# Performance work log

Measured on AMD Instinct MI355X. Metric: run time of the kernel, lower is better.

The kernel has to match this reference:

```python
import jax, jax.numpy as jnp
import numpy as np

H = 8          # num_heads
EPS = 1e-6     # layernorm epsilon
NEG_INF = -1e9


def _ln(x, g, b):
    m = jnp.mean(x, axis=-1, keepdims=True)
    v = jnp.mean(jnp.square(x - m), axis=-1, keepdims=True)
    return g * (x - m) * jax.lax.rsqrt(v + EPS) + b


def _mha(xq, kv, wq, wk, wv, wo, bias):
    # xq: [B,Tq,D], kv: [B,Tk,D]; weights [D,D]. Returns (out [B,Tq,D], weights [B,H,Tq,Tk]).
    B, Tq, D = xq.shape
    dh = D // H
    q = (xq @ wq) * (dh ** -0.5)
    k = kv @ wk
    v = kv @ wv
    q = q.reshape(B, Tq, H, dh).transpose(0, 2, 1, 3)
    k = k.reshape(B, -1, H, dh).transpose(0, 2, 1, 3)
    v = v.reshape(B, -1, H, dh).transpose(0, 2, 1, 3)
    logits = jnp.einsum('bhqd,bhkd->bhqk', q, k)
    if bias is not None:
        logits = logits + bias
    w = jax.nn.softmax(logits, axis=-1)
    out = jnp.einsum('bhqk,bhkd->bhqd', w, v).transpose(0, 2, 1, 3).reshape(B, Tq, D)
    return out @ wo, w


def setup_inputs() -> dict:
    key = jax.random.key(0)
    ks = jax.random.split(key, 16)
    B, Td, Te, D, F, L = 2, 2048, 2048, 512, 2048, 2
    s = 0.02
    inp = {
        'x': jax.random.normal(ks[0], (B, Td, D), jnp.float32),
        'enc_a': jax.random.normal(ks[1], (B, Te, D), jnp.float32),
        'enc_c': jax.random.normal(ks[2], (B, Te, D), jnp.float32),
        'sa_wq': jax.random.normal(ks[3], (L, D, D), jnp.float32) * s,
        'sa_wk': jax.random.normal(ks[4], (L, D, D), jnp.float32) * s,
        'sa_wv': jax.random.normal(ks[5], (L, D, D), jnp.float32) * s,
        'sa_wo': jax.random.normal(ks[6], (L, D, D), jnp.float32) * s,
        'ed_wq': jax.random.normal(ks[7], (L, D, D), jnp.float32) * s,
        'ed_wk': jax.random.normal(ks[8], (L, D, D), jnp.float32) * s,
        'ed_wv': jax.random.normal(ks[9], (L, D, D), jnp.float32) * s,
        'ed_wo': jax.random.normal(ks[10], (L, D, D), jnp.float32) * s,
        'ffn_w1': jax.random.normal(ks[11], (L, D, F), jnp.float32) * s,
        'ffn_w2': jax.random.normal(ks[12], (L, F, D), jnp.float32) * s,
        'ln1_g': jnp.ones((L, D), jnp.float32), 'ln1_b': jnp.zeros((L, D), jnp.float32),
        'ln2_g': jnp.ones((L, D), jnp.float32), 'ln2_b': jnp.zeros((L, D), jnp.float32),
        'ln3_g': jnp.ones((L, D), jnp.float32), 'ln3_b': jnp.zeros((L, D), jnp.float32),
        'out_g': jnp.ones((D,), jnp.float32), 'out_b': jnp.zeros((D,), jnp.float32),
    }
    return inp


def reference(x, enc_a, enc_c, sa_wq, sa_wk, sa_wv, sa_wo, ed_wq, ed_wk, ed_wv, ed_wo,
              ffn_w1, ffn_w2, ln1_g, ln1_b, ln2_g, ln2_b, ln3_g, ln3_b, out_g, out_b):
    B, T, D = x.shape
    L = sa_wq.shape[0]
    # decoder self-attention causal bias, broadcast over [B,H]
    causal = jnp.where(jnp.tril(jnp.ones((T, T), bool)), 0.0, NEG_INF)[None, None]
    avg = None
    for i in range(L):
        h = _ln(x, ln1_g[i], ln1_b[i])
        y, _ = _mha(h, h, sa_wq[i], sa_wk[i], sa_wv[i], sa_wo[i], causal)
        x = x + y  # residual (dropout inactive at eval)
        h = _ln(x, ln2_g[i], ln2_b[i])
        y0, _ = _mha(h, enc_a, ed_wq[i], ed_wk[i], ed_wv[i], ed_wo[i], None)
        y1, w = _mha(h, enc_c, ed_wq[i], ed_wk[i], ed_wv[i], ed_wo[i], None)
        # original overwrites attn_scores with second call's head-averaged weights
        scores = jnp.mean(w, axis=1) / L
        avg = scores if avg is None else avg + scores
        x = x + y0 + y1
        h = _ln(x, ln3_g[i], ln3_b[i])
        x = x + jax.nn.relu(h @ ffn_w1[i]) @ ffn_w2[i]
    x = _ln(x, out_g, out_b)
    return x, avg
```

## Files before the change

kernel.cpp:

```cpp
#include <hip/hip_runtime.h>
#include <hip/hip_bf16.h>

#define BB 2
#define TT 2048
#define DD 512
#define FF 2048
#define HH 8
#define DH 64
#define LL 2
#define MM (BB*TT)

typedef __attribute__((ext_vector_type(8))) short bf16x8;
typedef __attribute__((ext_vector_type(4))) float f32x4;

__device__ __forceinline__ float bf2f(unsigned short u) {
    return __uint_as_float(((unsigned int)u) << 16);
}
__device__ __forceinline__ unsigned short f2bf(float f) {
    unsigned int u = __float_as_uint(f);
    u += 0x7fffu + ((u >> 16) & 1u);
    return (unsigned short)(u >> 16);
}
__device__ __forceinline__ unsigned int cvtpk(float a, float b) {
    unsigned int r;
    asm("v_cvt_pk_bf16_f32 %0, %1, %2" : "=v"(r) : "v"(a), "v"(b));
    return r;
}
__device__ __forceinline__ void gload16(const void* g, void* l) {
    __builtin_amdgcn_global_load_lds((__attribute__((address_space(1))) void*)g,
                                     (__attribute__((address_space(3))) void*)l, 16, 0, 0);
}

template<bool BF16OUT>
__global__ __launch_bounds__(256) void ln_kernel(const float* __restrict__ x,
                                                 const float* __restrict__ g,
                                                 const float* __restrict__ b,
                                                 void* __restrict__ out)
{
    const int row = blockIdx.x;
    const int tid = threadIdx.x;
    const float2 v = ((const float2*)(x + (size_t)row * DD))[tid];
    float s = v.x + v.y;
    float q = v.x * v.x + v.y * v.y;
    #pragma unroll
    for (int off = 32; off; off >>= 1) {
        s += __shfl_down(s, off);
        q += __shfl_down(q, off);
    }
    __shared__ float ss[4], qq[4];
    const int wid = tid >> 6;
    if ((tid & 63) == 0) { ss[wid] = s; qq[wid] = q; }
    __syncthreads();
    s = ss[0] + ss[1] + ss[2] + ss[3];
    q = qq[0] + qq[1] + qq[2] + qq[3];
    const float mean = s * (1.0f / DD);
    const float var = q * (1.0f / DD) - mean * mean;
    const float inv = rsqrtf(var + 1e-6f);
    const float2 gg = ((const float2*)g)[tid];
    const float2 bb = ((const float2*)b)[tid];
    const float ox = gg.x * (v.x - mean) * inv + bb.x;
    const float oy = gg.y * (v.y - mean) * inv + bb.y;
    if (BF16OUT) {
        const unsigned int pk = cvtpk(ox, oy);
        ((unsigned int*)((unsigned short*)out + (size_t)row * DD))[tid] = pk;
    } else {
        float2 o; o.x = ox; o.y = oy;
        ((float2*)((float*)out + (size_t)row * DD))[tid] = o;
    }
}

struct CvtEJob { const float* s; unsigned short* d; };
struct CvtEJobs2 { CvtEJob j[2]; };

__global__ __launch_bounds__(256) void cvt_kernel(CvtEJobs2 P, int n)
{
    const CvtEJob jb = P.j[blockIdx.z];
    const int i = (blockIdx.x * 256 + threadIdx.x) * 8;
    if (i >= n) return;
    const float4 a = *(const float4*)(jb.s + i);
    const float4 b = *(const float4*)(jb.s + i + 4);
    unsigned int o[4];
    o[0] = cvtpk(a.x, a.y); o[1] = cvtpk(a.z, a.w);
    o[2] = cvtpk(b.x, b.y); o[3] = cvtpk(b.z, b.w);
    *(bf16x8*)(jb.d + i) = *(bf16x8*)o;
}

struct CvtTJob { const float* s; unsigned short* d; int K; int N; };
struct CvtTJobs20 { CvtTJob j[20]; };

__global__ __launch_bounds__(256) void cvtT_kernel(CvtTJobs20 P)
{
    __shared__ float t[32][33];
    const CvtTJob jb = P.j[blockIdx.z];
    const int gk = blockIdx.y << 5, gn = blockIdx.x << 5;
    if (gk >= jb.K || gn >= jb.N) return;
    const int tx = threadIdx.x & 31, ty = threadIdx.x >> 5;
    #pragma unroll
    for (int i = 0; i < 4; ++i)
        t[ty + i * 8][tx] = jb.s[(size_t)(gk + ty + i * 8) * jb.N + gn + tx];
    __syncthreads();
    #pragma unroll
    for (int i = 0; i < 4; ++i)
        jb.d[(size_t)(gn + ty + i * 8) * jb.K + gk + tx] = f2bf(t[tx][ty + i * 8]);
}

struct GemmJob {
    const unsigned short* A;
    const unsigned short* Wt;
    const float* res;
    float* Cf;
    unsigned short* Cb;
    unsigned short* Ct;
    float scale;
    int relu;
};
struct GemmJobs8 { GemmJob j[8]; };

__global__ __launch_bounds__(256, 2) void gemm_mfma(GemmJobs8 P, int M, int N, int K)
{
    __shared__ __align__(16) unsigned char lds[32768];
    const GemmJob jb = P.j[blockIdx.z];
    const int tid = threadIdx.x, lane = tid & 63, w = tid >> 6;
    const int bn = blockIdx.x << 7, bm = blockIdx.y << 7;
    const int wr = (w >> 1) << 6, wc = (w & 1) << 6;
    const size_t strA = (size_t)K * 2;

    f32x4 acc[4][4] = {};
    const int akey = (lane & 7) << 4;
    const int frow = lane & 15;
    const int kq = (lane >> 4) << 4;

    for (int kt = 0; kt < K; kt += 64) {
        __syncthreads();
        #pragma unroll
        for (int c = 0; c < 4; ++c) {
            const int q = c * 4 + w;
            const int o = (q << 10) + (lane << 4);
            const int row = o >> 7;
            const int colb = (o & 127) ^ ((row & 7) << 4);
            gload16((const char*)jb.A + (size_t)(bm + row) * strA + kt * 2 + colb,
                    lds + (q << 10));
            gload16((const char*)jb.Wt + (size_t)(bn + row) * strA + kt * 2 + colb,
                    lds + 16384 + (q << 10));
        }
        asm volatile("s_waitcnt vmcnt(0)" ::: "memory");
        __syncthreads();
        #pragma unroll
        for (int kk = 0; kk < 2; ++kk) {
            bf16x8 av[4], bv[4];
            #pragma unroll
            for (int i = 0; i < 4; ++i) {
                const int rA = wr + (i << 4) + frow;
                av[i] = *(const bf16x8*)(lds + (rA << 7) + ((((kk << 6) + kq)) ^ akey));
                const int rB = wc + (i << 4) + frow;
                bv[i] = *(const bf16x8*)(lds + 16384 + (rB << 7) + ((((kk << 6) + kq)) ^ akey));
            }
            #pragma unroll
            for (int i = 0; i < 4; ++i)
                #pragma unroll
                for (int j = 0; j < 4; ++j)
                    acc[i][j] = __builtin_amdgcn_mfma_f32_16x16x32_bf16(av[i], bv[j], acc[i][j], 0, 0, 0);
        }
    }

    const int crow0 = (lane >> 4) << 2;
    const int ccol = lane & 15;
    if (jb.Ct) {
        #pragma unroll
        for (int i = 0; i < 4; ++i)
            #pragma unroll
            for (int j = 0; j < 4; ++j) {
                const int gm = bm + wr + (i << 4) + crow0;
                const int gn = bn + wc + (j << 4) + ccol;
                const int bI = gm >> 11, t = gm & 2047;
                const int hI = gn >> 6, d = gn & 63;
                uint2 pk;
                pk.x = cvtpk(acc[i][j][0], acc[i][j][1]);
                pk.y = cvtpk(acc[i][j][2], acc[i][j][3]);
                *(uint2*)(jb.Ct + ((size_t)((bI * HH + hI) * DH + d)) * TT + t) = pk;
            }
        return;
    }
    #pragma unroll
    for (int i = 0; i < 4; ++i) {
        #pragma unroll
        for (int j = 0; j < 4; ++j) {
            #pragma unroll
            for (int r = 0; r < 4; ++r) {
                const int gm = bm + wr + (i << 4) + crow0 + r;
                const int gn = bn + wc + (j << 4) + ccol;
                float v = acc[i][j][r] * jb.scale;
                if (jb.relu) v = fmaxf(v, 0.f);
                const size_t idx = (size_t)gm * N + gn;
                if (jb.res) v += jb.res[idx];
                if (jb.Cf) jb.Cf[idx] = v;
                if (jb.Cb) jb.Cb[idx] = f2bf(v);
            }
        }
    }
}

template<bool CAUSAL, bool DUAL, int NQ>
__global__ __launch_bounds__(256, (NQ == 1) ? 4 : 3) void flash_mfma(
    const unsigned short* __restrict__ q,
    const unsigned short* __restrict__ ka, const unsigned short* __restrict__ vta,
    const unsigned short* __restrict__ kc, const unsigned short* __restrict__ vtc,
    unsigned short* __restrict__ Opart,
    float* __restrict__ mlpart)
{
    __shared__ __align__(16) char lds[(NQ == 1) ? 40960 : 49152];
    const int tid = threadIdx.x;
    const int lane = tid & 63, w = tid >> 6;
    const int g4 = lane >> 4, c = lane & 15;

    constexpr int GX = (32 / NQ) * 2;
    const int f = blockIdx.x + GX * (blockIdx.y + 8 * blockIdx.z);
    const int xcd = f & 7;
    const int tt = f >> 3;
    const int u = tt % GX;
    const int half = u & 1, jq = u >> 1;
    const int grp = (tt / GX) * 8 + xcd;
    int b, h, which;
    if (DUAL) { which = grp & 1; b = (grp >> 1) & 1; h = grp >> 2; }
    else      { which = 0;       b = grp & 1;        h = grp >> 1; }
    const int q0 = jq * (64 * NQ);
    const int q0w = q0 + w * (16 * NQ);
    const int kendw = q0w + 16 * NQ;

    const unsigned short* k  = (DUAL && which) ? kc : ka;
    const unsigned short* vt = (DUAL && which) ? vtc : vta;
    const int slot = (DUAL ? (which << 1) : 0) + half;
    unsigned short* Od = Opart + (size_t)slot * MM * DD;
    float* mld = mlpart + (size_t)slot * (BB * HH * TT * 2);

    bf16x8 Qf[NQ][2];
    #pragma unroll
    for (int jb = 0; jb < NQ; ++jb) {
        const unsigned short* qp = q + (size_t)(b * TT + q0w + (jb << 4) + c) * DD + h * DH + (g4 << 3);
        Qf[jb][0] = *(const bf16x8*)qp;
        Qf[jb][1] = *(const bf16x8*)(qp + 32);
    }
    const char* kbase = (const char*)(k + (size_t)b * TT * DD + h * DH);
    const char* vtb   = (const char*)(vt + (size_t)(b * HH + h) * DH * TT);
    char* Pw = lds + 32768 + w * (NQ * 2048);
    const int pkey = (c & 7) << 4;

    f32x4 O[NQ][4] = {};
    float lpart[NQ];
    #pragma unroll
    for (int jb = 0; jb < NQ; ++jb) lpart[jb] = 0.f;

    const int ntt = CAUSAL ? ((q0 + 64 * NQ) >> 6) : (TT >> 6);
    const int tBeg = half ? ((ntt + 1) >> 1) : 0;
    const int tEnd = half ? ntt : ((ntt + 1) >> 1);

    auto STAGE = [&](int t, int sel) {
        const int kt = t << 6;
        char* Kb = lds + sel * 8192;
        char* Vb = lds + 16384 + sel * 8192;
        #pragma unroll
        for (int c8 = 0; c8 < 2; ++c8) {
            const int qc = (c8 << 2) + w;
            const int o = (qc << 10) + (lane << 4);
            const int row = o >> 7;
            const int colb = (o & 127) ^ ((row & 7) << 4);
            gload16(kbase + (size_t)(kt + row) * (DD * 2) + colb, Kb + (qc << 10));
            gload16(vtb + (size_t)row * (TT * 2) + kt * 2 + colb, Vb + (qc << 10));
        }
    };

    if (tBeg < tEnd) {
        STAGE(tBeg, 0);
        asm volatile("s_waitcnt vmcnt(0)" ::: "memory");
        __syncthreads();

        for (int t = tBeg; t < tEnd; ++t) {
            const int cur = (t - tBeg) & 1;
            if (t + 1 < tEnd) STAGE(t + 1, cur ^ 1);
            const int kt = t << 6;

            if (!CAUSAL || kt < kendw) {
                const char* Kb = lds + cur * 8192;
                const char* Vb = lds + 16384 + cur * 8192;

                f32x4 s[NQ][4] = {};
                #pragma unroll
                for (int kk = 0; kk < 2; ++kk) {
                    bf16x8 av[4];
                    #pragma unroll
                    for (int i = 0; i < 4; ++i) {
                        const int r = (i << 4) + c;
                        av[i] = *(const bf16x8*)(Kb + (r << 7) + (((kk << 6) + (g4 << 4)) ^ ((r & 7) << 4)));
                    }
                    #pragma unroll
                    for (int i = 0; i < 4; ++i)
                        #pragma unroll
                        for (int jb = 0; jb < NQ; ++jb)
                            s[jb][i] = __builtin_amdgcn_mfma_f32_16x16x32_bf16(av[i], Qf[jb][kk], s[jb][i], 0, 0, 0);
                }

                #pragma unroll
                for (int jb = 0; jb < NQ; ++jb) {
                    const int qbase = q0w + (jb << 4);
                    if (CAUSAL && kt + 63 > qbase) {
                        #pragma unroll
                        for (int i = 0; i < 4; ++i)
                            #pragma unroll
                            for (int r = 0; r < 4; ++r)
                                if (kt + (i << 4) + (g4 << 2) + r > qbase + c) s[jb][i][r] = -1e30f;
                    }
                    float ps = 0.f;
                    #pragma unroll
                    for (int i = 0; i < 4; ++i)
                        #pragma unroll
                        for (int r = 0; r < 4; ++r) {
                            const float p = exp2f(s[jb][i][r]);
                            s[jb][i][r] = p;
                            ps += p;
                        }
                    lpart[jb] += ps;
                    #pragma unroll
                    for (int i = 0; i < 4; ++i) {
                        uint2 pk;
                        pk.x = cvtpk(s[jb][i][0], s[jb][i][1]);
                        pk.y = cvtpk(s[jb][i][2], s[jb][i][3]);
                        const int baddr = (((jb << 4) + c) << 7) + (((i << 4) + (g4 << 2)) << 1);
                        *(uint2*)(Pw + (baddr ^ pkey)) = pk;
                    }
                }
                asm volatile("s_waitcnt lgkmcnt(0)" ::: "memory");
                __builtin_amdgcn_sched_barrier(0);

                #pragma unroll
                for (int kk = 0; kk < 2; ++kk) {
                    bf16x8 pa[NQ];
                    #pragma unroll
                    for (int jb = 0; jb < NQ; ++jb)
                        pa[jb] = *(const bf16x8*)(Pw + (((((jb << 4) + c) << 7) + (kk << 6) + (g4 << 4)) ^ pkey));
                    #pragma unroll
                    for (int jj = 0; jj < 4; ++jj) {
                        const int d = (jj << 4) + c;
                        const bf16x8 vb = *(const bf16x8*)(Vb + (d << 7) + (((kk << 6) + (g4 << 4)) ^ ((d & 7) << 4)));
                        #pragma unroll
                        for (int jb = 0; jb < NQ; ++jb)
                            O[jb][jj] = __builtin_amdgcn_mfma_f32_16x16x32_bf16(pa[jb], vb, O[jb][jj], 0, 0, 0);
                    }
                }
            }

            asm volatile("s_waitcnt vmcnt(0)" ::: "memory");
            __syncthreads();
        }
    }

    #pragma unroll
    for (int jb = 0; jb < NQ; ++jb) {
        float l2 = lpart[jb] + __shfl_xor(lpart[jb], 16);
        const float ltot = l2 + __shfl_xor(l2, 32);
        #pragma unroll
        for (int jj = 0; jj < 4; ++jj)
            #pragma unroll
            for (int r = 0; r < 4; ++r) {
                const int qr = q0w + (jb << 4) + (g4 << 2) + r;
                Od[(size_t)(b * TT + qr) * DD + h * DH + (jj << 4) + c] = f2bf(O[jb][jj][r]);
            }
        if (lane < 16) {
            const size_t mi = (((size_t)b * HH + h) * TT + q0w + (jb << 4) + lane) * 2;
            mld[mi] = 0.f;
            mld[mi + 1] = ltot;
        }
    }
}

template<int NS>
__global__ __launch_bounds__(256) void merge_kernel(
    const unsigned short* __restrict__ Opart, const float* __restrict__ mlpart,
    unsigned short* __restrict__ out)
{
    const int row = blockIdx.x;
    const int b = row >> 11, rt = row & 2047;
    const int t = threadIdx.x;
    const int d0 = t << 1, h = d0 >> 6;
    float acc0 = 0.f, acc1 = 0.f;
    #pragma unroll
    for (int s = 0; s < NS; ++s) {
        const size_t mb = ((size_t)(b * HH + h) * TT + rt) * 2;
        const float* mp0 = mlpart + (size_t)(s * 2 + 0) * (BB * HH * TT * 2) + mb;
        const float* mp1 = mlpart + (size_t)(s * 2 + 1) * (BB * HH * TT * 2) + mb;
        const float m0 = mp0[0], l0 = mp0[1], m1 = mp1[0], l1 = mp1[1];
        const float M = fmaxf(m0, m1);
        const float a0 = exp2f(m0 - M), a1 = exp2f(m1 - M);
        const float inv = 1.f / (a0 * l0 + a1 * l1);
        const unsigned short* p0 = Opart + (size_t)(s * 2 + 0) * MM * DD + (size_t)row * DD + d0;
        const unsigned short* p1 = Opart + (size_t)(s * 2 + 1) * MM * DD + (size_t)row * DD + d0;
        acc0 += (a0 * bf2f(p0[0]) + a1 * bf2f(p1[0])) * inv;
        acc1 += (a0 * bf2f(p0[1]) + a1 * bf2f(p1[1])) * inv;
    }
    ((unsigned int*)(out + (size_t)row * DD))[t] = cvtpk(acc0, acc1);
}

__global__ __launch_bounds__(256) void avg_mfma_kernel(const unsigned short* __restrict__ qm,
                                                       const unsigned short* __restrict__ kcm,
                                                       const float* __restrict__ mlpart,
                                                       float* __restrict__ avg, int first)
{
    __shared__ __align__(16) unsigned char ldsQ[8192];
    __shared__ __align__(16) unsigned char ldsK[4][8192];
    __shared__ float sM[8][64];
    __shared__ float sIL[8][64];
    const int tid = threadIdx.x;
    const int lane = tid & 63, w = tid >> 6;

    const int f = blockIdx.x;
    const int xcd = f & 7, t = f >> 3;
    const int b = xcd >> 2;
    const int q0 = ((((xcd & 3) << 3) + (t >> 3))) << 6;
    const int kt0 = (((t & 7) << 2) + w) << 6;

    #pragma unroll
    for (int u = 0; u < 2; ++u) {
        const int e = (u << 8) + tid;
        const int h = e >> 6, r = e & 63;
        const size_t mb = ((size_t)(b * HH + h) * TT + q0 + r) * 2;
        const float* mp2 = mlpart + (size_t)2 * (BB * HH * TT * 2) + mb;
        const float* mp3 = mlpart + (size_t)3 * (BB * HH * TT * 2) + mb;
        const float m2 = mp2[0], l2v = mp2[1], m3 = mp3[0], l3v = mp3[1];
        const float M = fmaxf(m2, m3);
        const float L = exp2f(m2 - M) * l2v + exp2f(m3 - M) * l3v;
        sM[h][r] = M;
        sIL[h][r] = 1.f / L;
    }

    float avac[4][4][4] = {};
    const int akey = (lane & 7) << 4;
    const int frow = lane & 15;
    const int kq = (lane >> 4) << 4;
    const int crow0 = (lane >> 4) << 2;

    for (int h = 0; h < 8; ++h) {
        __syncthreads();
        #pragma unroll
        for (int u = 0; u < 2; ++u) {
            const int ch = (u << 2) + w;
            const int o = (ch << 10) + (lane << 4);
            const int row = o >> 7;
            const int colb = (o & 127) ^ ((row & 7) << 4);
            gload16((const char*)qm + ((size_t)(b * TT + q0 + row) * DD + h * DH) * 2 + colb,
                    ldsQ + (ch << 10));
        }
        #pragma unroll
        for (int c8 = 0; c8 < 8; ++c8) {
            const int o = (c8 << 10) + (lane << 4);
            const int row = o >> 7;
            const int colb = (o & 127) ^ ((row & 7) << 4);
            gload16((const char*)kcm + ((size_t)(b * TT + kt0 + row) * DD + h * DH) * 2 + colb,
                    &ldsK[w][c8 << 10]);
        }
        asm volatile("s_waitcnt vmcnt(0)" ::: "memory");
        __syncthreads();

        f32x4 s[4][4] = {};
        #pragma unroll
        for (int kk = 0; kk < 2; ++kk) {
            bf16x8 qv[4], kv[4];
            #pragma unroll
            for (int i = 0; i < 4; ++i) {
                qv[i] = *(const bf16x8*)(ldsQ + (((i << 4) + frow) << 7) + (((kk << 6) + kq) ^ akey));
                kv[i] = *(const bf16x8*)(&ldsK[w][(((i << 4) + frow) << 7) + (((kk << 6) + kq) ^ akey)]);
            }
            #pragma unroll
            for (int i = 0; i < 4; ++i)
                #pragma unroll
                for (int j = 0; j < 4; ++j)
                    s[i][j] = __builtin_amdgcn_mfma_f32_16x16x32_bf16(qv[i], kv[j], s[i][j], 0, 0, 0);
        }
        #pragma unroll
        for (int i = 0; i < 4; ++i)
            #pragma unroll
            for (int j = 0; j < 4; ++j)
                #pragma unroll
                for (int r = 0; r < 4; ++r) {
                    const int qr = (i << 4) + crow0 + r;
                    avac[i][j][r] += exp2f(s[i][j][r] - sM[h][qr]) * sIL[h][qr];
                }
    }

    float* dst = avg + ((size_t)b * TT + q0) * TT + kt0;
    #pragma unroll
    for (int i = 0; i < 4; ++i)
        #pragma unroll
        for (int j = 0; j < 4; ++j)
            #pragma unroll
            for (int r = 0; r < 4; ++r) {
                const int qr = (i << 4) + crow0 + r;
                const int kc = (j << 4) + (lane & 15);
                const float v = avac[i][j][r] * (1.f / (HH * LL));
                float* p = dst + (size_t)qr * TT + kc;
                *p = first ? v : (*p + v);
            }
}

extern "C" void kernel_launch(void* const* d_in, const int* in_sizes, int n_in,
                              void* d_out, int out_size, void* d_ws, size_t ws_size,
                              hipStream_t stream)
{
    const float* x_in   = (const float*)d_in[0];
    const float* enc_a  = (const float*)d_in[1];
    const float* enc_c  = (const float*)d_in[2];
    const float* sa_wq0 = (const float*)d_in[3];
    const float* sa_wk0 = (const float*)d_in[4];
    const float* sa_wv0 = (const float*)d_in[5];
    const float* sa_wo0 = (const float*)d_in[6];
    const float* ed_wq0 = (const float*)d_in[7];
    const float* ed_wk0 = (const float*)d_in[8];
    const float* ed_wv0 = (const float*)d_in[9];
    const float* ed_wo0 = (const float*)d_in[10];
    const float* ffn_w10 = (const float*)d_in[11];
    const float* ffn_w20 = (const float*)d_in[12];
    const float* ln1_g0 = (const float*)d_in[13];
    const float* ln1_b0 = (const float*)d_in[14];
    const float* ln2_g0 = (const float*)d_in[15];
    const float* ln2_b0 = (const float*)d_in[16];
    const float* ln3_g0 = (const float*)d_in[17];
    const float* ln3_b0 = (const float*)d_in[18];
    const float* out_g  = (const float*)d_in[19];
    const float* out_b  = (const float*)d_in[20];

    const size_t NTD = (size_t)MM * DD;
    const size_t MB = 1u << 20;
    char* W = (char*)d_ws;
    float*          x_buf   = (float*)(W);
    unsigned short* h_bf    = (unsigned short*)(W + 8 * MB);
    unsigned short* q_bf    = (unsigned short*)(W + 12 * MB);
    unsigned short* k1_bf   = (unsigned short*)(W + 16 * MB);
    unsigned short* vt1     = (unsigned short*)(W + 20 * MB);
    unsigned short* k2_bf   = (unsigned short*)(W + 24 * MB);
    unsigned short* vt2     = (unsigned short*)(W + 28 * MB);
    unsigned short* attnA   = (unsigned short*)(W + 32 * MB);
    unsigned short* attnS   = (unsigned short*)(W + 36 * MB);
    unsigned short* encA_bf = (unsigned short*)(W + 41 * MB);
    unsigned short* encC_bf = (unsigned short*)(W + 45 * MB);
    unsigned short* wbf     = (unsigned short*)(W + 49 * MB);
    unsigned short* Opart   = (unsigned short*)(W + 68 * MB);
    float*          mlpart  = (float*)(W + 84 * MB);
    unsigned short* ffn_bf  = q_bf;

    unsigned short* w1t = wbf + (size_t)16 * DD * DD;
    unsigned short* w2t = w1t + (size_t)2 * DD * FF;
    auto wd = [&](int l, int which) { return wbf + ((size_t)(l * 8 + which)) * DD * DD; };

    float* x_out   = (float*)d_out;
    float* avg_out = (float*)d_out + NTD;

    hipMemcpyAsync(x_buf, x_in, NTD * sizeof(float), hipMemcpyDeviceToDevice, stream);

    {
        CvtTJobs20 J{};
        const float* srcs[8] = {sa_wq0, sa_wk0, sa_wv0, sa_wo0, ed_wq0, ed_wk0, ed_wv0, ed_wo0};
        for (int l = 0; l < LL; ++l)
            for (int t = 0; t < 8; ++t)
                J.j[l * 8 + t] = {srcs[t] + (size_t)l * DD * DD, wd(l, t), DD, DD};
        for (int l = 0; l < LL; ++l) {
            J.j[16 + l] = {ffn_w10 + (size_t)l * DD * FF, w1t + (size_t)l * FF * DD, DD, FF};
            J.j[18 + l] = {ffn_w20 + (size_t)l * FF * DD, w2t + (size_t)l * DD * FF, FF, DD};
        }
        cvtT_kernel<<<dim3(FF / 32, FF / 32, 20), 256, 0, stream>>>(J);
    }
    {
        CvtEJobs2 J{};
        J.j[0] = {enc_a, encA_bf};
        J.j[1] = {enc_c, encC_bf};
        cvt_kernel<<<dim3(NTD / 8 / 256, 1, 2), 256, 0, stream>>>(J, (int)NTD);
    }

    const dim3 flashSelfG(64, HH, BB);
    const dim3 flashCrossG(32, HH, BB * 2);
    const float qscale = 0.125f * 1.4426950408889634f;

    for (int i = 0; i < LL; ++i) {
        const size_t fOff = (size_t)i * DD * FF;
        const size_t lOff = (size_t)i * DD;

        ln_kernel<true><<<MM, 256, 0, stream>>>(x_buf, ln1_g0 + lOff, ln1_b0 + lOff, h_bf);
        {
            GemmJobs8 J{};
            J.j[0] = {h_bf, wd(i, 0), nullptr, nullptr, q_bf, nullptr, qscale, 0};
            J.j[1] = {h_bf, wd(i, 1), nullptr, nullptr, k1_bf, nullptr, 1.f, 0};
            J.j[2] = {h_bf, wd(i, 2), nullptr, nullptr, nullptr, vt1, 1.f, 0};
            gemm_mfma<<<dim3(DD / 128, MM / 128, 3), 256, 0, stream>>>(J, MM, DD, DD);
        }
        flash_mfma<true, false, 1><<<flashSelfG, 256, 0, stream>>>(
            q_bf, k1_bf, vt1, nullptr, nullptr, Opart, mlpart);
        merge_kernel<1><<<MM, 256, 0, stream>>>(Opart, mlpart, attnA);
        {
            GemmJobs8 J{};
            J.j[0] = {attnA, wd(i, 3), x_buf, x_buf, nullptr, nullptr, 1.f, 0};
            gemm_mfma<<<dim3(DD / 128, MM / 128, 1), 256, 0, stream>>>(J, MM, DD, DD);
        }

        ln_kernel<true><<<MM, 256, 0, stream>>>(x_buf, ln2_g0 + lOff, ln2_b0 + lOff, h_bf);
        {
            GemmJobs8 J{};
            J.j[0] = {h_bf,    wd(i, 4), nullptr, nullptr, q_bf, nullptr, qscale, 0};
            J.j[1] = {encA_bf, wd(i, 5), nullptr, nullptr, k1_bf, nullptr, 1.f, 0};
            J.j[2] = {encA_bf, wd(i, 6), nullptr, nullptr, nullptr, vt1, 1.f, 0};
            J.j[3] = {encC_bf, wd(i, 5), nullptr, nullptr, k2_bf, nullptr, 1.f, 0};
            J.j[4] = {encC_bf, wd(i, 6), nullptr, nullptr, nullptr, vt2, 1.f, 0};
            gemm_mfma<<<dim3(DD / 128, MM / 128, 5), 256, 0, stream>>>(J, MM, DD, DD);
        }
        flash_mfma<false, true, 2><<<flashCrossG, 256, 0, stream>>>(
            q_bf, k1_bf, vt1, k2_bf, vt2, Opart, mlpart);
        merge_kernel<2><<<MM, 256, 0, stream>>>(Opart, mlpart, attnS);
        avg_mfma_kernel<<<512, 256, 0, stream>>>(q_bf, k2_bf, mlpart, avg_out, (i == 0) ? 1 : 0);
        {
            GemmJobs8 J{};
            J.j[0] = {attnS, wd(i, 7), x_buf, x_buf, nullptr, nullptr, 1.f, 0};
            gemm_mfma<<<dim3(DD / 128, MM / 128, 1), 256, 0, stream>>>(J, MM, DD, DD);
        }

        ln_kernel<true><<<MM, 256, 0, stream>>>(x_buf, ln3_g0 + lOff, ln3_b0 + lOff, h_bf);
        {
            GemmJobs8 J{};
            J.j[0] = {h_bf, w1t + fOff, nullptr, nullptr, ffn_bf, nullptr, 1.f, 1};
            gemm_mfma<<<dim3(FF / 128, MM / 128, 1), 256, 0, stream>>>(J, MM, FF, DD);
        }
        {
            GemmJobs8 J{};
            J.j[0] = {ffn_bf, w2t + fOff, x_buf, x_buf, nullptr, nullptr, 1.f, 0};
            gemm_mfma<<<dim3(DD / 128, MM / 128, 1), 256, 0, stream>>>(J, MM, DD, FF);
        }
    }

    ln_kernel<false><<<MM, 256, 0, stream>>>(x_buf, out_g, out_b, x_out);
}
```

Measured before the change: 663.7 us.

## Split head-averaged attention kernel across head groups with atomic accumulation

Restructures the attention-weight averaging kernel from 512 blocks of four waves into 4096 single-wave blocks. Each block now handles one 64x64 query/key tile for a group of four heads, so the block-wide barriers and shared Q staging across waves go away. Partial results from the two head groups and the two layers are combined with float atomic adds into an output that is zeroed once up front with a memset. This raises parallelism and removes the first-layer branch, at the cost of a 32MB memset, doubled atomic traffic to the output, and reloading Q separately per wave.

```diff
diff --git a/kernel.cpp b/kernel.cpp
--- a/kernel.cpp
+++ b/kernel.cpp
@@ -399,36 +399,38 @@
     ((unsigned int*)(out + (size_t)row * DD))[t] = cvtpk(acc0, acc1);
 }
 
-__global__ __launch_bounds__(256) void avg_mfma_kernel(const unsigned short* __restrict__ qm,
-                                                       const unsigned short* __restrict__ kcm,
-                                                       const float* __restrict__ mlpart,
-                                                       float* __restrict__ avg, int first)
+__global__ __launch_bounds__(64) void avg_mfma_kernel(const unsigned short* __restrict__ qm,
+                                                      const unsigned short* __restrict__ kcm,
+                                                      const float* __restrict__ mlpart,
+                                                      float* __restrict__ avg)
 {
     __shared__ __align__(16) unsigned char ldsQ[8192];
-    __shared__ __align__(16) unsigned char ldsK[4][8192];
-    __shared__ float sM[8][64];
-    __shared__ float sIL[8][64];
-    const int tid = threadIdx.x;
-    const int lane = tid & 63, w = tid >> 6;
+    __shared__ __align__(16) unsigned char ldsK[8192];
+    __shared__ float sM[4][64];
+    __shared__ float sIL[4][64];
+    const int lane = threadIdx.x;
 
     const int f = blockIdx.x;
-    const int xcd = f & 7, t = f >> 3;
+    const int xcd = f & 7, rest = f >> 3;
     const int b = xcd >> 2;
-    const int q0 = ((((xcd & 3) << 3) + (t >> 3))) << 6;
-    const int kt0 = (((t & 7) << 2) + w) << 6;
-
-    #pragma unroll
-    for (int u = 0; u < 2; ++u) {
-        const int e = (u << 8) + tid;
-        const int h = e >> 6, r = e & 63;
-        const size_t mb = ((size_t)(b * HH + h) * TT + q0 + r) * 2;
+    const int hg = rest & 1;
+    const int qp = (rest >> 1) & 7;
+    const int ktg = rest >> 4;
+    const int q0 = (((xcd & 3) << 3) + qp) << 6;
+    const int kt0 = ktg << 6;
+    const int h0 = hg << 2;
+
+    #pragma unroll
+    for (int u = 0; u < 4; ++u) {
+        const int h = h0 + u;
+        const size_t mb = ((size_t)(b * HH + h) * TT + q0 + lane) * 2;
         const float* mp2 = mlpart + (size_t)2 * (BB * HH * TT * 2) + mb;
         const float* mp3 = mlpart + (size_t)3 * (BB * HH * TT * 2) + mb;
         const float m2 = mp2[0], l2v = mp2[1], m3 = mp3[0], l3v = mp3[1];
         const float M = fmaxf(m2, m3);
         const float L = exp2f(m2 - M) * l2v + exp2f(m3 - M) * l3v;
-        sM[h][r] = M;
-        sIL[h][r] = 1.f / L;
+        sM[u][lane] = M;
+        sIL[u][lane] = 1.f / L;
     }
 
     float avac[4][4][4] = {};
@@ -437,27 +439,26 @@
     const int kq = (lane >> 4) << 4;
     const int crow0 = (lane >> 4) << 2;
 
-    for (int h = 0; h < 8; ++h) {
-        __syncthreads();
-        #pragma unroll
-        for (int u = 0; u < 2; ++u) {
-            const int ch = (u << 2) + w;
-            const int o = (ch << 10) + (lane << 4);
-            const int row = o >> 7;
-            const int colb = (o & 127) ^ ((row & 7) << 4);
-            gload16((const char*)qm + ((size_t)(b * TT + q0 + row) * DD + h * DH) * 2 + colb,
-                    ldsQ + (ch << 10));
-        }
+    auto STAGE = [&](int u) {
+        const int h = h0 + u;
         #pragma unroll
         for (int c8 = 0; c8 < 8; ++c8) {
             const int o = (c8 << 10) + (lane << 4);
             const int row = o >> 7;
             const int colb = (o & 127) ^ ((row & 7) << 4);
+            gload16((const char*)qm + ((size_t)(b * TT + q0 + row) * DD + h * DH) * 2 + colb,
+                    ldsQ + (c8 << 10));
             gload16((const char*)kcm + ((size_t)(b * TT + kt0 + row) * DD + h * DH) * 2 + colb,
-                    &ldsK[w][c8 << 10]);
-        }
+                    ldsK + (c8 << 10));
+        }
+    };
+
+    for (int u = 0; u < 4; ++u) {
+        asm volatile("s_waitcnt lgkmcnt(0)" ::: "memory");
+        __builtin_amdgcn_sched_barrier(0);
+        STAGE(u);
         asm volatile("s_waitcnt vmcnt(0)" ::: "memory");
-        __syncthreads();
+        __builtin_amdgcn_sched_barrier(0);
 
         f32x4 s[4][4] = {};
         #pragma unroll
@@ -466,7 +467,7 @@
             #pragma unroll
             for (int i = 0; i < 4; ++i) {
                 qv[i] = *(const bf16x8*)(ldsQ + (((i << 4) + frow) << 7) + (((kk << 6) + kq) ^ akey));
-                kv[i] = *(const bf16x8*)(&ldsK[w][(((i << 4) + frow) << 7) + (((kk << 6) + kq) ^ akey)]);
+                kv[i] = *(const bf16x8*)(ldsK + (((i << 4) + frow) << 7) + (((kk << 6) + kq) ^ akey));
             }
             #pragma unroll
             for (int i = 0; i < 4; ++i)
@@ -481,7 +482,7 @@
                 #pragma unroll
                 for (int r = 0; r < 4; ++r) {
                     const int qr = (i << 4) + crow0 + r;
-                    avac[i][j][r] += exp2f(s[i][j][r] - sM[h][qr]) * sIL[h][qr];
+                    avac[i][j][r] += exp2f(s[i][j][r] - sM[u][qr]) * sIL[u][qr];
                 }
     }
 
@@ -494,9 +495,8 @@
             for (int r = 0; r < 4; ++r) {
                 const int qr = (i << 4) + crow0 + r;
                 const int kc = (j << 4) + (lane & 15);
-                const float v = avac[i][j][r] * (1.f / (HH * LL));
-                float* p = dst + (size_t)qr * TT + kc;
-                *p = first ? v : (*p + v);
+                unsafeAtomicAdd(dst + (size_t)qr * TT + kc,
+                                avac[i][j][r] * (1.f / (HH * LL)));
             }
 }
 
@@ -553,6 +553,7 @@
     float* avg_out = (float*)d_out + NTD;
 
     hipMemcpyAsync(x_buf, x_in, NTD * sizeof(float), hipMemcpyDeviceToDevice, stream);
+    hipMemsetAsync(avg_out, 0, (size_t)BB * TT * TT * sizeof(float), stream);
 
     {
         CvtTJobs20 J{};
@@ -611,7 +612,7 @@
         flash_mfma<false, true, 2><<<flashCrossG, 256, 0, stream>>>(
             q_bf, k1_bf, vt1, k2_bf, vt2, Opart, mlpart);
         merge_kernel<2><<<MM, 256, 0, stream>>>(Opart, mlpart, attnS);
-        avg_mfma_kernel<<<512, 256, 0, stream>>>(q_bf, k2_bf, mlpart, avg_out, (i == 0) ? 1 : 0);
+        avg_mfma_kernel<<<4096, 64, 0, stream>>>(q_bf, k2_bf, mlpart, avg_out);
         {
             GemmJobs8 J{};
             J.j[0] = {attnS, wd(i, 7), x_buf, x_buf, nullptr, nullptr, 1.f, 0};
```

Result: slower. 704.5 us (+6.1%).

## Defer cross-attention weight averaging to one final kernel over both layers

Applied to the files above, without the earlier changes.

Rather than running the head-averaged attention-weight kernel once per layer with a read-modify-write on the 32MB avg output, the per-layer cross-attention Q, K and softmax stats are stashed in the avg output buffer. At the end they are copied to workspace and a single kernel loops over all 16 layer-head pairs, writing avg once. This removes one full read and one write of the large avg tensor. In exchange it adds a 17MB device copy and per-layer stat copies, and relies on the output buffer as temporary storage.

```diff
diff --git a/kernel.cpp b/kernel.cpp
--- a/kernel.cpp
+++ b/kernel.cpp
@@ -399,15 +399,13 @@
     ((unsigned int*)(out + (size_t)row * DD))[t] = cvtpk(acc0, acc1);
 }
 
-__global__ __launch_bounds__(256) void avg_mfma_kernel(const unsigned short* __restrict__ qm,
-                                                       const unsigned short* __restrict__ kcm,
-                                                       const float* __restrict__ mlpart,
-                                                       float* __restrict__ avg, int first)
+__global__ __launch_bounds__(256) void avg_final_kernel(const unsigned short* __restrict__ stash,
+                                                        float* __restrict__ avg)
 {
     __shared__ __align__(16) unsigned char ldsQ[8192];
     __shared__ __align__(16) unsigned char ldsK[4][8192];
-    __shared__ float sM[8][64];
-    __shared__ float sIL[8][64];
+    __shared__ float sM[16][64];
+    __shared__ float sIL[16][64];
     const int tid = threadIdx.x;
     const int lane = tid & 63, w = tid >> 6;
 
@@ -417,18 +415,21 @@
     const int q0 = ((((xcd & 3) << 3) + (t >> 3))) << 6;
     const int kt0 = (((t & 7) << 2) + w) << 6;
 
-    #pragma unroll
-    for (int u = 0; u < 2; ++u) {
-        const int e = (u << 8) + tid;
-        const int h = e >> 6, r = e & 63;
+    const float* mlF = (const float*)(stash + (size_t)8 * 1024 * 1024);
+
+    #pragma unroll
+    for (int e4 = 0; e4 < 4; ++e4) {
+        const int e = (e4 << 8) + tid;
+        const int u = e >> 6, r = e & 63;
+        const int l = u >> 3, h = u & 7;
+        const float* mlL = mlF + (size_t)l * 131072;
         const size_t mb = ((size_t)(b * HH + h) * TT + q0 + r) * 2;
-        const float* mp2 = mlpart + (size_t)2 * (BB * HH * TT * 2) + mb;
-        const float* mp3 = mlpart + (size_t)3 * (BB * HH * TT * 2) + mb;
-        const float m2 = mp2[0], l2v = mp2[1], m3 = mp3[0], l3v = mp3[1];
+        const float m2 = mlL[mb], l2v = mlL[mb + 1];
+        const float m3 = mlL[65536 + mb], l3v = mlL[65536 + mb + 1];
         const float M = fmaxf(m2, m3);
         const float L = exp2f(m2 - M) * l2v + exp2f(m3 - M) * l3v;
-        sM[h][r] = M;
-        sIL[h][r] = 1.f / L;
+        sM[u][r] = M;
+        sIL[u][r] = 1.f / L;
     }
 
     float avac[4][4][4] = {};
@@ -437,15 +438,18 @@
     const int kq = (lane >> 4) << 4;
     const int crow0 = (lane >> 4) << 2;
 
-    for (int h = 0; h < 8; ++h) {
+    for (int u = 0; u < 16; ++u) {
+        const int l = u >> 3, h = u & 7;
+        const char* qm  = (const char*)(stash + (size_t)l * 2097152);
+        const char* kcm = (const char*)(stash + (size_t)(4194304 + l * 2097152));
         __syncthreads();
         #pragma unroll
-        for (int u = 0; u < 2; ++u) {
-            const int ch = (u << 2) + w;
+        for (int u2 = 0; u2 < 2; ++u2) {
+            const int ch = (u2 << 2) + w;
             const int o = (ch << 10) + (lane << 4);
             const int row = o >> 7;
             const int colb = (o & 127) ^ ((row & 7) << 4);
-            gload16((const char*)qm + ((size_t)(b * TT + q0 + row) * DD + h * DH) * 2 + colb,
+            gload16(qm + ((size_t)(b * TT + q0 + row) * DD + h * DH) * 2 + colb,
                     ldsQ + (ch << 10));
         }
         #pragma unroll
@@ -453,7 +457,7 @@
             const int o = (c8 << 10) + (lane << 4);
             const int row = o >> 7;
             const int colb = (o & 127) ^ ((row & 7) << 4);
-            gload16((const char*)kcm + ((size_t)(b * TT + kt0 + row) * DD + h * DH) * 2 + colb,
+            gload16(kcm + ((size_t)(b * TT + kt0 + row) * DD + h * DH) * 2 + colb,
                     &ldsK[w][c8 << 10]);
         }
         asm volatile("s_waitcnt vmcnt(0)" ::: "memory");
@@ -481,7 +485,7 @@
                 #pragma unroll
                 for (int r = 0; r < 4; ++r) {
                     const int qr = (i << 4) + crow0 + r;
-                    avac[i][j][r] += exp2f(s[i][j][r] - sM[h][qr]) * sIL[h][qr];
+                    avac[i][j][r] += exp2f(s[i][j][r] - sM[u][qr]) * sIL[u][qr];
                 }
     }
 
@@ -494,9 +498,7 @@
             for (int r = 0; r < 4; ++r) {
                 const int qr = (i << 4) + crow0 + r;
                 const int kc = (j << 4) + (lane & 15);
-                const float v = avac[i][j][r] * (1.f / (HH * LL));
-                float* p = dst + (size_t)qr * TT + kc;
-                *p = first ? v : (*p + v);
+                dst[(size_t)qr * TT + kc] = avac[i][j][r] * (1.f / (HH * LL));
             }
 }
 
@@ -552,6 +554,12 @@
     float* x_out   = (float*)d_out;
     float* avg_out = (float*)d_out + NTD;
 
+    char* stash = (char*)avg_out;
+    auto qs  = [&](int l) { return (unsigned short*)(stash + (size_t)l * 4 * MB); };
+    auto k2s = [&](int l) { return (unsigned short*)(stash + (size_t)(8 + 4 * l) * MB); };
+    auto mls = [&](int l) { return (float*)(stash + 16 * MB + (size_t)l * 512 * 1024); };
+    unsigned short* stashF = (unsigned short*)(W + 68 * MB);
+
     hipMemcpyAsync(x_buf, x_in, NTD * sizeof(float), hipMemcpyDeviceToDevice, stream);
 
     {
@@ -601,17 +609,18 @@
         ln_kernel<true><<<MM, 256, 0, stream>>>(x_buf, ln2_g0 + lOff, ln2_b0 + lOff, h_bf);
         {
             GemmJobs8 J{};
-            J.j[0] = {h_bf,    wd(i, 4), nullptr, nullptr, q_bf, nullptr, qscale, 0};
+            J.j[0] = {h_bf,    wd(i, 4), nullptr, nullptr, qs(i), nullptr, qscale, 0};
             J.j[1] = {encA_bf, wd(i, 5), nullptr, nullptr, k1_bf, nullptr, 1.f, 0};
             J.j[2] = {encA_bf, wd(i, 6), nullptr, nullptr, nullptr, vt1, 1.f, 0};
-            J.j[3] = {encC_bf, wd(i, 5), nullptr, nullptr, k2_bf, nullptr, 1.f, 0};
+            J.j[3] = {encC_bf, wd(i, 5), nullptr, nullptr, k2s(i), nullptr, 1.f, 0};
             J.j[4] = {encC_bf, wd(i, 6), nullptr, nullptr, nullptr, vt2, 1.f, 0};
             gemm_mfma<<<dim3(DD / 128, MM / 128, 5), 256, 0, stream>>>(J, MM, DD, DD);
         }
         flash_mfma<false, true, 2><<<flashCrossG, 256, 0, stream>>>(
-            q_bf, k1_bf, vt1, k2_bf, vt2, Opart, mlpart);
+            qs(i), k1_bf, vt1, k2s(i), vt2, Opart, mlpart);
         merge_kernel<2><<<MM, 256, 0, stream>>>(Opart, mlpart, attnS);
-        avg_mfma_kernel<<<512, 256, 0, stream>>>(q_bf, k2_bf, mlpart, avg_out, (i == 0) ? 1 : 0);
+        hipMemcpyAsync(mls(i), mlpart + (size_t)2 * (BB * HH * TT * 2),
+                       512 * 1024, hipMemcpyDeviceToDevice, stream);
         {
             GemmJobs8 J{};
             J.j[0] = {attnS, wd(i, 7), x_buf, x_buf, nullptr, nullptr, 1.f, 0};
@@ -631,5 +640,7 @@
         }
     }
 
+    hipMemcpyAsync(stashF, stash, (size_t)17 * MB, hipMemcpyDeviceToDevice, stream);
+    avg_final_kernel<<<512, 256, 0, stream>>>(stashF, avg_out);
     ln_kernel<false><<<MM, 256, 0, stream>>>(x_buf, out_g, out_b, x_out);
 }
```

New measurement: 620.6 us. 6.5% less time.
